# Kernel optimization log

Hardware: AMD Instinct MI355X
Metric: run time of the kernel (lower is better)

The kernel has to match this reference:

```python
import jax, jax.numpy as jnp
import numpy as np

Q_SIZE, K_SIZE, H = 256, 256, 128
N, n, m, D_V = 4, 512, 512, 256

def setup_inputs() -> dict:
    key = jax.random.key(0)
    k1, k2, k3, k4, k5, k6 = jax.random.split(key, 6)
    return {
        "query": jax.random.normal(k1, (N, n, Q_SIZE), dtype=jnp.float32),
        "key": jax.random.normal(k2, (N, m, K_SIZE), dtype=jnp.float32),
        "value": jax.random.normal(k3, (N, m, D_V), dtype=jnp.float32),
        "W_q": jax.random.normal(k4, (Q_SIZE, H), dtype=jnp.float32) / np.sqrt(Q_SIZE),
        "W_k": jax.random.normal(k5, (K_SIZE, H), dtype=jnp.float32) / np.sqrt(K_SIZE),
        "W_v": jax.random.normal(k6, (H,), dtype=jnp.float32) / np.sqrt(H),
    }

def reference(query, key, value, W_q, W_k, W_v):
    q = query @ W_q                      # (N, n, h)
    k = key @ W_k                        # (N, m, h)
    # broadcast additive scores: tanh((N,n,1,h) + (N,1,m,h)) reduced by W_v -> (N,n,m)
    feats = jnp.tanh(q[:, :, None, :] + k[:, None, :, :])
    scores = jnp.einsum('bnmh,h->bnm', feats, W_v)
    attn = jax.nn.softmax(scores, axis=-1)  # softmax over keys m
    return jnp.einsum('bnm,bmd->bnd', attn, value)
```

## Files before the change

### kernel.cpp

```cpp
#include <hip/hip_runtime.h>
#include <math.h>

#define NB   4
#define SEQN 512
#define SEQM 512
#define QS   256
#define HH   128
#define DV   256
#define BM   (NB * SEQM)

static constexpr float kPreScale = 2.8853900817779268f;
static constexpr float kLog2e    = 1.4426950408889634f;

#if __has_builtin(__builtin_amdgcn_exp2f)
__device__ __forceinline__ float fexp2(float x) { return __builtin_amdgcn_exp2f(x); }
#else
__device__ __forceinline__ float fexp2(float x) { return exp2f(x); }
#endif

#if __has_builtin(__builtin_amdgcn_rcpf)
__device__ __forceinline__ float frcp(float x) { return __builtin_amdgcn_rcpf(x); }
#else
__device__ __forceinline__ float frcp(float x) { return 1.0f / x; }
#endif

__global__ __launch_bounds__(256) void proj_kernel(
    const float* __restrict__ query, const float* __restrict__ key,
    const float* __restrict__ Wq, const float* __restrict__ Wk,
    const float* __restrict__ wv,
    float* __restrict__ qt, float2* __restrict__ kt) {
  const int t = threadIdx.x;
  const int half = (NB * SEQN) / 8;
  const bool isK = blockIdx.x >= half;
  const int rb   = isK ? (blockIdx.x - half) : blockIdx.x;
  const float* __restrict__ in = isK ? key : query;
  const float* __restrict__ W  = isK ? Wk  : Wq;
  const int row0 = rb * 8;

  const int j  = t & 127;
  const int r0 = __builtin_amdgcn_readfirstlane((t >> 7) * 4);

  const float* __restrict__ x0p = in + (size_t)(row0 + r0 + 0) * QS;
  const float* __restrict__ x1p = in + (size_t)(row0 + r0 + 1) * QS;
  const float* __restrict__ x2p = in + (size_t)(row0 + r0 + 2) * QS;
  const float* __restrict__ x3p = in + (size_t)(row0 + r0 + 3) * QS;

  float a0 = 0.f, a1 = 0.f, a2 = 0.f, a3 = 0.f;
  for (int k0 = 0; k0 < QS; k0 += 4) {
    const float w0 = W[(k0 + 0) * HH + j];
    const float w1 = W[(k0 + 1) * HH + j];
    const float w2 = W[(k0 + 2) * HH + j];
    const float w3 = W[(k0 + 3) * HH + j];
    const float4 x0 = *reinterpret_cast<const float4*>(x0p + k0);
    const float4 x1 = *reinterpret_cast<const float4*>(x1p + k0);
    const float4 x2 = *reinterpret_cast<const float4*>(x2p + k0);
    const float4 x3 = *reinterpret_cast<const float4*>(x3p + k0);
    a0 = fmaf(x0.x, w0, fmaf(x0.y, w1, fmaf(x0.z, w2, fmaf(x0.w, w3, a0))));
    a1 = fmaf(x1.x, w0, fmaf(x1.y, w1, fmaf(x1.z, w2, fmaf(x1.w, w3, a1))));
    a2 = fmaf(x2.x, w0, fmaf(x2.y, w1, fmaf(x2.z, w2, fmaf(x2.w, w3, a2))));
    a3 = fmaf(x3.x, w0, fmaf(x3.y, w1, fmaf(x3.z, w2, fmaf(x3.w, w3, a3))));
  }
  const float wvj = wv[j];
  float acc[4] = {a0, a1, a2, a3};
#pragma unroll
  for (int r = 0; r < 4; ++r) {
    const float e  = fexp2(acc[r] * kPreScale);
    const float rc = frcp(e + 1.0f);
    float A = fmaf(-2.0f, rc, 1.0f);
    A = fminf(fmaxf(A, -0.99999988f), 0.99999988f);
    const int grow = row0 + r0 + r;
    if (isK) {
      kt[(size_t)j * BM + grow] = make_float2(A, wvj * A);
    } else {
      qt[(size_t)grow * (2 * HH) + j]      = A;
      qt[(size_t)grow * (2 * HH) + HH + j] = wvj * A;
    }
  }
}

__global__ __launch_bounds__(512) void fused_kernel(
    const float* __restrict__ qt, const float2* __restrict__ kt,
    const float* __restrict__ value, float* __restrict__ out) {
  __shared__ float sp[4][SEQM];
  __shared__ float pvbuf[8][4][DV];
  __shared__ float wred[16];

  const int t  = threadIdx.x;
  const int b  = blockIdx.x >> 7;
  const int n0 = (blockIdx.x & 127) * 4;
  const int m  = t;

  const float* __restrict__ qb = qt + ((size_t)b * SEQN + n0) * (2 * HH);
  const float2* __restrict__ kb = kt + (size_t)b * SEQM + m;

  float N[4], D[4];
#pragma unroll
  for (int n = 0; n < 4; ++n) { N[n] = 0.f; D[n] = 1.f; }

  for (int h0 = 0; h0 < HH; h0 += 8) {
    float kA[8], kW[8];
#pragma unroll
    for (int jj = 0; jj < 8; ++jj) {
      const float2 f = kb[(size_t)(h0 + jj) * BM];
      kA[jj] = f.x; kW[jj] = f.y;
    }
#pragma unroll
    for (int n = 0; n < 4; ++n) {
      const float* qr = qb + n * (2 * HH);
      const float4 a0 = *reinterpret_cast<const float4*>(qr + h0);
      const float4 a1 = *reinterpret_cast<const float4*>(qr + h0 + 4);
      const float4 v0 = *reinterpret_cast<const float4*>(qr + HH + h0);
      const float4 v1 = *reinterpret_cast<const float4*>(qr + HH + h0 + 4);
      const float s0 = v0.x + kW[0], d0 = fmaf(a0.x, kA[0], 1.0f);
      const float s1 = v0.y + kW[1], d1 = fmaf(a0.y, kA[1], 1.0f);
      const float s2 = v0.z + kW[2], d2 = fmaf(a0.z, kA[2], 1.0f);
      const float s3 = v0.w + kW[3], d3 = fmaf(a0.w, kA[3], 1.0f);
      const float s4 = v1.x + kW[4], d4 = fmaf(a1.x, kA[4], 1.0f);
      const float s5 = v1.y + kW[5], d5 = fmaf(a1.y, kA[5], 1.0f);
      const float s6 = v1.z + kW[6], d6 = fmaf(a1.z, kA[6], 1.0f);
      const float s7 = v1.w + kW[7], d7 = fmaf(a1.w, kA[7], 1.0f);
      const float t01 = fmaf(s0, d1, s1 * d0), e01 = d0 * d1;
      const float t23 = fmaf(s2, d3, s3 * d2), e23 = d2 * d3;
      const float t45 = fmaf(s4, d5, s5 * d4), e45 = d4 * d5;
      const float t67 = fmaf(s6, d7, s7 * d6), e67 = d6 * d7;
      const float t03 = fmaf(t01, e23, t23 * e01), e03 = e01 * e23;
      const float t47 = fmaf(t45, e67, t67 * e45), e47 = e45 * e67;
      const float t07 = fmaf(t03, e47, t47 * e03), e07 = e03 * e47;
      N[n] = fmaf(N[n], e07, t07 * D[n]);
      D[n] *= e07;
    }
  }
#pragma unroll
  for (int n = 0; n < 4; ++n) sp[n][m] = N[n] * frcp(D[n]);
  __syncthreads();

  const int wave = t >> 6;
  const int lane = t & 63;
  const int row  = wave & 3;
  const int hv   = wave >> 2;
  float v[4];
  float mx = -1e30f;
#pragma unroll
  for (int i = 0; i < 4; ++i) {
    v[i] = sp[row][hv * 256 + lane + 64 * i];
    mx = fmaxf(mx, v[i]);
  }
#pragma unroll
  for (int off = 32; off > 0; off >>= 1) mx = fmaxf(mx, __shfl_xor(mx, off));
  if (lane == 0) wred[wave] = mx;
  __syncthreads();
  mx = fmaxf(wred[row], wred[row + 4]);
  float sum = 0.f;
#pragma unroll
  for (int i = 0; i < 4; ++i) {
    const float p = fexp2((v[i] - mx) * kLog2e);
    sum += p;
    sp[row][hv * 256 + lane + 64 * i] = p;
  }
#pragma unroll
  for (int off = 32; off > 0; off >>= 1) sum += __shfl_xor(sum, off);
  if (lane == 0) wred[8 + wave] = sum;
  __syncthreads();

  const float* __restrict__ vb = value + (size_t)b * SEQM * DV;
  const int dq = (t & 63) * 4;
  const int mg = t >> 6;
  float o[4][4];
#pragma unroll
  for (int n = 0; n < 4; ++n)
#pragma unroll
    for (int jj = 0; jj < 4; ++jj) o[n][jj] = 0.f;
  const int mbeg = mg * 64;
  for (int mi = 0; mi < 64; mi += 4) {
    const int m0 = mbeg + mi;
    const float4 vv0 = *reinterpret_cast<const float4*>(vb + (size_t)(m0 + 0) * DV + dq);
    const float4 vv1 = *reinterpret_cast<const float4*>(vb + (size_t)(m0 + 1) * DV + dq);
    const float4 vv2 = *reinterpret_cast<const float4*>(vb + (size_t)(m0 + 2) * DV + dq);
    const float4 vv3 = *reinterpret_cast<const float4*>(vb + (size_t)(m0 + 3) * DV + dq);
#pragma unroll
    for (int n = 0; n < 4; ++n) {
      const float4 p4 = *reinterpret_cast<const float4*>(&sp[n][m0]);
      o[n][0] = fmaf(p4.x, vv0.x, fmaf(p4.y, vv1.x, fmaf(p4.z, vv2.x, fmaf(p4.w, vv3.x, o[n][0]))));
      o[n][1] = fmaf(p4.x, vv0.y, fmaf(p4.y, vv1.y, fmaf(p4.z, vv2.y, fmaf(p4.w, vv3.y, o[n][1]))));
      o[n][2] = fmaf(p4.x, vv0.z, fmaf(p4.y, vv1.z, fmaf(p4.z, vv2.z, fmaf(p4.w, vv3.z, o[n][2]))));
      o[n][3] = fmaf(p4.x, vv0.w, fmaf(p4.y, vv1.w, fmaf(p4.z, vv2.w, fmaf(p4.w, vv3.w, o[n][3]))));
    }
  }
#pragma unroll
  for (int n = 0; n < 4; ++n)
    *reinterpret_cast<float4*>(&pvbuf[mg][n][dq]) =
        make_float4(o[n][0], o[n][1], o[n][2], o[n][3]);
  __syncthreads();

  {
    const int cn    = wave & 3;
    const int dbase = (wave >> 2) * 128;
    const float rsn = frcp(wred[8 + cn] + wred[8 + cn + 4]);
    const size_t ob = ((size_t)b * SEQN + n0 + cn) * DV;
#pragma unroll
    for (int k2 = 0; k2 < 2; ++k2) {
      const int d = dbase + k2 * 64 + lane;
      float acc = 0.f;
#pragma unroll
      for (int g = 0; g < 8; ++g) acc += pvbuf[g][cn][d];
      out[ob + d] = acc * rsn;
    }
  }
}

extern "C" void kernel_launch(void* const* d_in, const int* in_sizes, int n_in,
                              void* d_out, int out_size, void* d_ws, size_t ws_size,
                              hipStream_t stream) {
  const float* query = (const float*)d_in[0];
  const float* key   = (const float*)d_in[1];
  const float* value = (const float*)d_in[2];
  const float* W_q   = (const float*)d_in[3];
  const float* W_k   = (const float*)d_in[4];
  const float* W_v   = (const float*)d_in[5];
  float* out = (float*)d_out;

  float*  qt = (float*)d_out;
  float2* kt = (float2*)d_ws;

  proj_kernel<<<2 * (NB * SEQN) / 8, 256, 0, stream>>>(query, key, W_q, W_k, W_v, qt, kt);
  fused_kernel<<<NB * (SEQN / 4), 512, 0, stream>>>(qt, kt, value, out);
}
```

Baseline: 52.63 us.

## Double threads per block by splitting hidden dim and rows across more threads

The fused kernel now runs 1024 threads per block. Each half of the block handles half of the hidden dimension, and the two partial rational numerator/denominator pairs are combined through shared memory. The softmax and PV stages are re-split across 16 waves, with a two-step reduction that reuses a shared-memory union. The projection kernel also moves to 512 threads, with each thread computing 2 rows instead of 4. The aim is more parallelism per block and shorter serial chains per thread, at the cost of extra synchronisation and less reuse of weight loads in the projection.

```diff
diff --git a/kernel.cpp b/kernel.cpp
--- a/kernel.cpp
+++ b/kernel.cpp
@@ -24,7 +24,7 @@
 __device__ __forceinline__ float frcp(float x) { return 1.0f / x; }
 #endif
 
-__global__ __launch_bounds__(256) void proj_kernel(
+__global__ __launch_bounds__(512) void proj_kernel(
     const float* __restrict__ query, const float* __restrict__ key,
     const float* __restrict__ Wq, const float* __restrict__ Wk,
     const float* __restrict__ wv,
@@ -38,14 +38,12 @@
   const int row0 = rb * 8;
 
   const int j  = t & 127;
-  const int r0 = __builtin_amdgcn_readfirstlane((t >> 7) * 4);
+  const int r0 = __builtin_amdgcn_readfirstlane((t >> 7) * 2);
 
   const float* __restrict__ x0p = in + (size_t)(row0 + r0 + 0) * QS;
   const float* __restrict__ x1p = in + (size_t)(row0 + r0 + 1) * QS;
-  const float* __restrict__ x2p = in + (size_t)(row0 + r0 + 2) * QS;
-  const float* __restrict__ x3p = in + (size_t)(row0 + r0 + 3) * QS;
-
-  float a0 = 0.f, a1 = 0.f, a2 = 0.f, a3 = 0.f;
+
+  float a0 = 0.f, a1 = 0.f;
   for (int k0 = 0; k0 < QS; k0 += 4) {
     const float w0 = W[(k0 + 0) * HH + j];
     const float w1 = W[(k0 + 1) * HH + j];
@@ -53,17 +51,13 @@
     const float w3 = W[(k0 + 3) * HH + j];
     const float4 x0 = *reinterpret_cast<const float4*>(x0p + k0);
     const float4 x1 = *reinterpret_cast<const float4*>(x1p + k0);
-    const float4 x2 = *reinterpret_cast<const float4*>(x2p + k0);
-    const float4 x3 = *reinterpret_cast<const float4*>(x3p + k0);
     a0 = fmaf(x0.x, w0, fmaf(x0.y, w1, fmaf(x0.z, w2, fmaf(x0.w, w3, a0))));
     a1 = fmaf(x1.x, w0, fmaf(x1.y, w1, fmaf(x1.z, w2, fmaf(x1.w, w3, a1))));
-    a2 = fmaf(x2.x, w0, fmaf(x2.y, w1, fmaf(x2.z, w2, fmaf(x2.w, w3, a2))));
-    a3 = fmaf(x3.x, w0, fmaf(x3.y, w1, fmaf(x3.z, w2, fmaf(x3.w, w3, a3))));
   }
   const float wvj = wv[j];
-  float acc[4] = {a0, a1, a2, a3};
-#pragma unroll
-  for (int r = 0; r < 4; ++r) {
+  float acc[2] = {a0, a1};
+#pragma unroll
+  for (int r = 0; r < 2; ++r) {
     const float e  = fexp2(acc[r] * kPreScale);
     const float rc = frcp(e + 1.0f);
     float A = fmaf(-2.0f, rc, 1.0f);
@@ -78,17 +72,21 @@
   }
 }
 
-__global__ __launch_bounds__(512) void fused_kernel(
+__global__ __launch_bounds__(1024) void fused_kernel(
     const float* __restrict__ qt, const float2* __restrict__ kt,
     const float* __restrict__ value, float* __restrict__ out) {
+  __shared__ union SMem {
+    float2 nd[2][4][SEQM];
+    float  pv[8][4][DV];
+  } u;
   __shared__ float sp[4][SEQM];
-  __shared__ float pvbuf[8][4][DV];
-  __shared__ float wred[16];
+  __shared__ float wred[32];
 
   const int t  = threadIdx.x;
   const int b  = blockIdx.x >> 7;
   const int n0 = (blockIdx.x & 127) * 4;
-  const int m  = t;
+  const int m  = t & 511;
+  const int hbase = (t >> 9) * 64;
 
   const float* __restrict__ qb = qt + ((size_t)b * SEQN + n0) * (2 * HH);
   const float2* __restrict__ kb = kt + (size_t)b * SEQM + m;
@@ -97,7 +95,7 @@
 #pragma unroll
   for (int n = 0; n < 4; ++n) { N[n] = 0.f; D[n] = 1.f; }
 
-  for (int h0 = 0; h0 < HH; h0 += 8) {
+  for (int h0 = hbase; h0 < hbase + 64; h0 += 8) {
     float kA[8], kW[8];
 #pragma unroll
     for (int jj = 0; jj < 8; ++jj) {
@@ -131,35 +129,44 @@
     }
   }
 #pragma unroll
-  for (int n = 0; n < 4; ++n) sp[n][m] = N[n] * frcp(D[n]);
+  for (int n = 0; n < 4; ++n) u.nd[t >> 9][n][m] = make_float2(N[n], D[n]);
+  __syncthreads();
+
+  {
+    const int nsel = (t >> 9) * 2;
+#pragma unroll
+    for (int k2 = 0; k2 < 2; ++k2) {
+      const int n = nsel + k2;
+      const float2 f1 = u.nd[0][n][m];
+      const float2 f2 = u.nd[1][n][m];
+      const float Nt = fmaf(f1.x, f2.y, f2.x * f1.y);
+      const float Dt = f1.y * f2.y;
+      sp[n][m] = Nt * frcp(Dt);
+    }
+  }
   __syncthreads();
 
   const int wave = t >> 6;
   const int lane = t & 63;
   const int row  = wave & 3;
-  const int hv   = wave >> 2;
-  float v[4];
-  float mx = -1e30f;
-#pragma unroll
-  for (int i = 0; i < 4; ++i) {
-    v[i] = sp[row][hv * 256 + lane + 64 * i];
-    mx = fmaxf(mx, v[i]);
-  }
+  const int qtr  = wave >> 2;
+  const int sbase = qtr * 128 + lane;
+  float v0 = sp[row][sbase];
+  float v1 = sp[row][sbase + 64];
+  float mx = fmaxf(v0, v1);
 #pragma unroll
   for (int off = 32; off > 0; off >>= 1) mx = fmaxf(mx, __shfl_xor(mx, off));
   if (lane == 0) wred[wave] = mx;
   __syncthreads();
-  mx = fmaxf(wred[row], wred[row + 4]);
-  float sum = 0.f;
-#pragma unroll
-  for (int i = 0; i < 4; ++i) {
-    const float p = fexp2((v[i] - mx) * kLog2e);
-    sum += p;
-    sp[row][hv * 256 + lane + 64 * i] = p;
-  }
+  mx = fmaxf(fmaxf(wred[row], wred[row + 4]), fmaxf(wred[row + 8], wred[row + 12]));
+  const float p0 = fexp2((v0 - mx) * kLog2e);
+  const float p1 = fexp2((v1 - mx) * kLog2e);
+  sp[row][sbase]      = p0;
+  sp[row][sbase + 64] = p1;
+  float sum = p0 + p1;
 #pragma unroll
   for (int off = 32; off > 0; off >>= 1) sum += __shfl_xor(sum, off);
-  if (lane == 0) wred[8 + wave] = sum;
+  if (lane == 0) wred[16 + wave] = sum;
   __syncthreads();
 
   const float* __restrict__ vb = value + (size_t)b * SEQM * DV;
@@ -170,8 +177,8 @@
   for (int n = 0; n < 4; ++n)
 #pragma unroll
     for (int jj = 0; jj < 4; ++jj) o[n][jj] = 0.f;
-  const int mbeg = mg * 64;
-  for (int mi = 0; mi < 64; mi += 4) {
+  const int mbeg = mg * 32;
+  for (int mi = 0; mi < 32; mi += 4) {
     const int m0 = mbeg + mi;
     const float4 vv0 = *reinterpret_cast<const float4*>(vb + (size_t)(m0 + 0) * DV + dq);
     const float4 vv1 = *reinterpret_cast<const float4*>(vb + (size_t)(m0 + 1) * DV + dq);
@@ -186,25 +193,31 @@
       o[n][3] = fmaf(p4.x, vv0.w, fmaf(p4.y, vv1.w, fmaf(p4.z, vv2.w, fmaf(p4.w, vv3.w, o[n][3]))));
     }
   }
-#pragma unroll
-  for (int n = 0; n < 4; ++n)
-    *reinterpret_cast<float4*>(&pvbuf[mg][n][dq]) =
-        make_float4(o[n][0], o[n][1], o[n][2], o[n][3]);
+  if (mg >= 8) {
+#pragma unroll
+    for (int n = 0; n < 4; ++n)
+      *reinterpret_cast<float4*>(&u.pv[mg - 8][n][dq]) =
+          make_float4(o[n][0], o[n][1], o[n][2], o[n][3]);
+  }
+  __syncthreads();
+  if (mg < 8) {
+#pragma unroll
+    for (int n = 0; n < 4; ++n) {
+      float4 prev = *reinterpret_cast<const float4*>(&u.pv[mg][n][dq]);
+      prev.x += o[n][0]; prev.y += o[n][1]; prev.z += o[n][2]; prev.w += o[n][3];
+      *reinterpret_cast<float4*>(&u.pv[mg][n][dq]) = prev;
+    }
+  }
   __syncthreads();
 
   {
-    const int cn    = wave & 3;
-    const int dbase = (wave >> 2) * 128;
-    const float rsn = frcp(wred[8 + cn] + wred[8 + cn + 4]);
-    const size_t ob = ((size_t)b * SEQN + n0 + cn) * DV;
-#pragma unroll
-    for (int k2 = 0; k2 < 2; ++k2) {
-      const int d = dbase + k2 * 64 + lane;
-      float acc = 0.f;
-#pragma unroll
-      for (int g = 0; g < 8; ++g) acc += pvbuf[g][cn][d];
-      out[ob + d] = acc * rsn;
-    }
+    const int n = t >> 8;
+    const int d = t & 255;
+    const float rsn = frcp(wred[16 + n] + wred[20 + n] + wred[24 + n] + wred[28 + n]);
+    float acc = 0.f;
+#pragma unroll
+    for (int g = 0; g < 8; ++g) acc += u.pv[g][n][d];
+    out[((size_t)b * SEQN + n0 + n) * DV + d] = acc * rsn;
   }
 }
 
@@ -222,6 +235,6 @@
   float*  qt = (float*)d_out;
   float2* kt = (float2*)d_ws;
 
-  proj_kernel<<<2 * (NB * SEQN) / 8, 256, 0, stream>>>(query, key, W_q, W_k, W_v, qt, kt);
-  fused_kernel<<<NB * (SEQN / 4), 512, 0, stream>>>(qt, kt, value, out);
+  proj_kernel<<<2 * (NB * SEQN) / 8, 512, 0, stream>>>(query, key, W_q, W_k, W_v, qt, kt);
+  fused_kernel<<<NB * (SEQN / 4), 1024, 0, stream>>>(qt, kt, value, out);
 }
```

Result: slower. 78.44 us (+49.0%).

## Double fused-kernel rows per block, prefetch key tiles, widen projection blocks

Applied to the files above, without the earlier changes.

The fused kernel now handles 8 query rows per 1024-thread block, in two 512-thread halves, so each block loads each value row once for 8 outputs instead of 4. The next 8 key features are prefetched into registers during the current h-step. Each softmax row is now reduced by a single wave, which removes the cross-wave max/sum exchange, and the partial PV sums are combined in two LDS stages. The projection kernel uses 512 threads with 2 rows per thread instead of 4, which raises parallelism. The trade-offs are fewer blocks in flight (256 instead of 512), higher register pressure under a 1024-thread launch bound, and an extra barrier.

```diff
diff --git a/kernel.cpp b/kernel.cpp
--- a/kernel.cpp
+++ b/kernel.cpp
@@ -24,7 +24,7 @@
 __device__ __forceinline__ float frcp(float x) { return 1.0f / x; }
 #endif
 
-__global__ __launch_bounds__(256) void proj_kernel(
+__global__ __launch_bounds__(512) void proj_kernel(
     const float* __restrict__ query, const float* __restrict__ key,
     const float* __restrict__ Wq, const float* __restrict__ Wk,
     const float* __restrict__ wv,
@@ -38,14 +38,12 @@
   const int row0 = rb * 8;
 
   const int j  = t & 127;
-  const int r0 = __builtin_amdgcn_readfirstlane((t >> 7) * 4);
+  const int r0 = __builtin_amdgcn_readfirstlane((t >> 7) * 2);
 
   const float* __restrict__ x0p = in + (size_t)(row0 + r0 + 0) * QS;
   const float* __restrict__ x1p = in + (size_t)(row0 + r0 + 1) * QS;
-  const float* __restrict__ x2p = in + (size_t)(row0 + r0 + 2) * QS;
-  const float* __restrict__ x3p = in + (size_t)(row0 + r0 + 3) * QS;
-
-  float a0 = 0.f, a1 = 0.f, a2 = 0.f, a3 = 0.f;
+
+  float a0 = 0.f, a1 = 0.f;
   for (int k0 = 0; k0 < QS; k0 += 4) {
     const float w0 = W[(k0 + 0) * HH + j];
     const float w1 = W[(k0 + 1) * HH + j];
@@ -53,17 +51,13 @@
     const float w3 = W[(k0 + 3) * HH + j];
     const float4 x0 = *reinterpret_cast<const float4*>(x0p + k0);
     const float4 x1 = *reinterpret_cast<const float4*>(x1p + k0);
-    const float4 x2 = *reinterpret_cast<const float4*>(x2p + k0);
-    const float4 x3 = *reinterpret_cast<const float4*>(x3p + k0);
     a0 = fmaf(x0.x, w0, fmaf(x0.y, w1, fmaf(x0.z, w2, fmaf(x0.w, w3, a0))));
     a1 = fmaf(x1.x, w0, fmaf(x1.y, w1, fmaf(x1.z, w2, fmaf(x1.w, w3, a1))));
-    a2 = fmaf(x2.x, w0, fmaf(x2.y, w1, fmaf(x2.z, w2, fmaf(x2.w, w3, a2))));
-    a3 = fmaf(x3.x, w0, fmaf(x3.y, w1, fmaf(x3.z, w2, fmaf(x3.w, w3, a3))));
   }
   const float wvj = wv[j];
-  float acc[4] = {a0, a1, a2, a3};
-#pragma unroll
-  for (int r = 0; r < 4; ++r) {
+  float acc[2] = {a0, a1};
+#pragma unroll
+  for (int r = 0; r < 2; ++r) {
     const float e  = fexp2(acc[r] * kPreScale);
     const float rc = frcp(e + 1.0f);
     float A = fmaf(-2.0f, rc, 1.0f);
@@ -78,31 +72,37 @@
   }
 }
 
-__global__ __launch_bounds__(512) void fused_kernel(
+__global__ __launch_bounds__(1024) void fused_kernel(
     const float* __restrict__ qt, const float2* __restrict__ kt,
     const float* __restrict__ value, float* __restrict__ out) {
-  __shared__ float sp[4][SEQM];
-  __shared__ float pvbuf[8][4][DV];
-  __shared__ float wred[16];
+  __shared__ float sp[8][SEQM];
+  __shared__ float pvbuf[4][8][DV];
+  __shared__ float rsh[8];
 
   const int t  = threadIdx.x;
-  const int b  = blockIdx.x >> 7;
-  const int n0 = (blockIdx.x & 127) * 4;
-  const int m  = t;
-
-  const float* __restrict__ qb = qt + ((size_t)b * SEQN + n0) * (2 * HH);
+  const int b  = blockIdx.x >> 6;
+  const int n0 = (blockIdx.x & 63) * 8;
+  const int m  = t & 511;
+  const int nq4 = __builtin_amdgcn_readfirstlane((t >> 9) * 4);
+
+  const float* __restrict__ qb = qt + ((size_t)b * SEQN + n0 + nq4) * (2 * HH);
   const float2* __restrict__ kb = kt + (size_t)b * SEQM + m;
 
   float N[4], D[4];
 #pragma unroll
   for (int n = 0; n < 4; ++n) { N[n] = 0.f; D[n] = 1.f; }
+
+  float2 fb[8];
+#pragma unroll
+  for (int jj = 0; jj < 8; ++jj) fb[jj] = kb[(size_t)jj * BM];
 
   for (int h0 = 0; h0 < HH; h0 += 8) {
     float kA[8], kW[8];
 #pragma unroll
-    for (int jj = 0; jj < 8; ++jj) {
-      const float2 f = kb[(size_t)(h0 + jj) * BM];
-      kA[jj] = f.x; kW[jj] = f.y;
+    for (int jj = 0; jj < 8; ++jj) { kA[jj] = fb[jj].x; kW[jj] = fb[jj].y; }
+    if (h0 + 8 < HH) {
+#pragma unroll
+      for (int jj = 0; jj < 8; ++jj) fb[jj] = kb[(size_t)(h0 + 8 + jj) * BM];
     }
 #pragma unroll
     for (int n = 0; n < 4; ++n) {
@@ -131,80 +131,86 @@
     }
   }
 #pragma unroll
-  for (int n = 0; n < 4; ++n) sp[n][m] = N[n] * frcp(D[n]);
+  for (int n = 0; n < 4; ++n) sp[nq4 + n][m] = N[n] * frcp(D[n]);
   __syncthreads();
 
   const int wave = t >> 6;
   const int lane = t & 63;
-  const int row  = wave & 3;
-  const int hv   = wave >> 2;
-  float v[4];
+  const int row  = wave >> 1;
+  const int hf   = wave & 1;
+  float v[8];
   float mx = -1e30f;
 #pragma unroll
-  for (int i = 0; i < 4; ++i) {
-    v[i] = sp[row][hv * 256 + lane + 64 * i];
+  for (int i = 0; i < 8; ++i) {
+    v[i] = sp[row][lane + 64 * i];
     mx = fmaxf(mx, v[i]);
   }
 #pragma unroll
   for (int off = 32; off > 0; off >>= 1) mx = fmaxf(mx, __shfl_xor(mx, off));
-  if (lane == 0) wred[wave] = mx;
-  __syncthreads();
-  mx = fmaxf(wred[row], wred[row + 4]);
+  float p[8];
   float sum = 0.f;
 #pragma unroll
-  for (int i = 0; i < 4; ++i) {
-    const float p = fexp2((v[i] - mx) * kLog2e);
-    sum += p;
-    sp[row][hv * 256 + lane + 64 * i] = p;
+  for (int i = 0; i < 8; ++i) {
+    p[i] = fexp2((v[i] - mx) * kLog2e);
+    sum += p[i];
   }
 #pragma unroll
   for (int off = 32; off > 0; off >>= 1) sum += __shfl_xor(sum, off);
-  if (lane == 0) wred[8 + wave] = sum;
+  __syncthreads();
+#pragma unroll
+  for (int i = 4 * hf; i < 4 * hf + 4; ++i) sp[row][lane + 64 * i] = p[i];
+  if (hf == 0 && lane == 0) rsh[row] = frcp(sum);
   __syncthreads();
 
   const float* __restrict__ vb = value + (size_t)b * SEQM * DV;
-  const int dq = (t & 63) * 4;
-  const int mg = t >> 6;
-  float o[4][4];
-#pragma unroll
-  for (int n = 0; n < 4; ++n)
-#pragma unroll
-    for (int jj = 0; jj < 4; ++jj) o[n][jj] = 0.f;
+  const int dp = (t & 127) * 2;
+  const int mg = t >> 7;
+  float o[8][2];
+#pragma unroll
+  for (int n = 0; n < 8; ++n) { o[n][0] = 0.f; o[n][1] = 0.f; }
   const int mbeg = mg * 64;
   for (int mi = 0; mi < 64; mi += 4) {
     const int m0 = mbeg + mi;
-    const float4 vv0 = *reinterpret_cast<const float4*>(vb + (size_t)(m0 + 0) * DV + dq);
-    const float4 vv1 = *reinterpret_cast<const float4*>(vb + (size_t)(m0 + 1) * DV + dq);
-    const float4 vv2 = *reinterpret_cast<const float4*>(vb + (size_t)(m0 + 2) * DV + dq);
-    const float4 vv3 = *reinterpret_cast<const float4*>(vb + (size_t)(m0 + 3) * DV + dq);
-#pragma unroll
-    for (int n = 0; n < 4; ++n) {
+    const float2 w0 = *reinterpret_cast<const float2*>(vb + (size_t)(m0 + 0) * DV + dp);
+    const float2 w1 = *reinterpret_cast<const float2*>(vb + (size_t)(m0 + 1) * DV + dp);
+    const float2 w2 = *reinterpret_cast<const float2*>(vb + (size_t)(m0 + 2) * DV + dp);
+    const float2 w3 = *reinterpret_cast<const float2*>(vb + (size_t)(m0 + 3) * DV + dp);
+#pragma unroll
+    for (int n = 0; n < 8; ++n) {
       const float4 p4 = *reinterpret_cast<const float4*>(&sp[n][m0]);
-      o[n][0] = fmaf(p4.x, vv0.x, fmaf(p4.y, vv1.x, fmaf(p4.z, vv2.x, fmaf(p4.w, vv3.x, o[n][0]))));
-      o[n][1] = fmaf(p4.x, vv0.y, fmaf(p4.y, vv1.y, fmaf(p4.z, vv2.y, fmaf(p4.w, vv3.y, o[n][1]))));
-      o[n][2] = fmaf(p4.x, vv0.z, fmaf(p4.y, vv1.z, fmaf(p4.z, vv2.z, fmaf(p4.w, vv3.z, o[n][2]))));
-      o[n][3] = fmaf(p4.x, vv0.w, fmaf(p4.y, vv1.w, fmaf(p4.z, vv2.w, fmaf(p4.w, vv3.w, o[n][3]))));
-    }
-  }
-#pragma unroll
-  for (int n = 0; n < 4; ++n)
-    *reinterpret_cast<float4*>(&pvbuf[mg][n][dq]) =
-        make_float4(o[n][0], o[n][1], o[n][2], o[n][3]);
+      o[n][0] = fmaf(p4.x, w0.x, fmaf(p4.y, w1.x, fmaf(p4.z, w2.x, fmaf(p4.w, w3.x, o[n][0]))));
+      o[n][1] = fmaf(p4.x, w0.y, fmaf(p4.y, w1.y, fmaf(p4.z, w2.y, fmaf(p4.w, w3.y, o[n][1]))));
+    }
+  }
+  if (mg >= 4) {
+#pragma unroll
+    for (int n = 0; n < 8; ++n)
+      *reinterpret_cast<float2*>(&pvbuf[mg - 4][n][dp]) = make_float2(o[n][0], o[n][1]);
+  }
+  __syncthreads();
+  if (mg < 4) {
+#pragma unroll
+    for (int n = 0; n < 8; ++n) {
+      float2 prev = *reinterpret_cast<const float2*>(&pvbuf[mg][n][dp]);
+      prev.x += o[n][0]; prev.y += o[n][1];
+      *reinterpret_cast<float2*>(&pvbuf[mg][n][dp]) = prev;
+    }
+  }
   __syncthreads();
 
   {
-    const int cn    = wave & 3;
-    const int dbase = (wave >> 2) * 128;
-    const float rsn = frcp(wred[8 + cn] + wred[8 + cn + 4]);
-    const size_t ob = ((size_t)b * SEQN + n0 + cn) * DV;
-#pragma unroll
-    for (int k2 = 0; k2 < 2; ++k2) {
-      const int d = dbase + k2 * 64 + lane;
-      float acc = 0.f;
-#pragma unroll
-      for (int g = 0; g < 8; ++g) acc += pvbuf[g][cn][d];
-      out[ob + d] = acc * rsn;
-    }
+    const int n = t >> 7;
+    const int d = t & 127;
+    const float rsn = rsh[n];
+    float accA = 0.f, accB = 0.f;
+#pragma unroll
+    for (int g = 0; g < 4; ++g) {
+      accA += pvbuf[g][n][d];
+      accB += pvbuf[g][n][d + 128];
+    }
+    const size_t ob = ((size_t)b * SEQN + n0 + n) * DV;
+    out[ob + d]       = accA * rsn;
+    out[ob + d + 128] = accB * rsn;
   }
 }
 
@@ -222,6 +228,6 @@
   float*  qt = (float*)d_out;
   float2* kt = (float2*)d_ws;
 
-  proj_kernel<<<2 * (NB * SEQN) / 8, 256, 0, stream>>>(query, key, W_q, W_k, W_v, qt, kt);
-  fused_kernel<<<NB * (SEQN / 4), 512, 0, stream>>>(qt, kt, value, out);
+  proj_kernel<<<2 * (NB * SEQN) / 8, 512, 0, stream>>>(query, key, W_q, W_k, W_v, qt, kt);
+  fused_kernel<<<NB * (SEQN / 8), 1024, 0, stream>>>(qt, kt, value, out);
 }
```

Measured after the change: 48.03 us. 1.1x faster.
